# Optimization experiments

Hardware: AMD Instinct MI355X
Metric: run time of the kernel (lower is better)

Reference implementation:

```python
import jax, jax.numpy as jnp
from jax import lax
import numpy as np

B, C, H, W = 2, 256, 256, 256
NH, P = 8, 4
D = C // NH
EPS_BN = 1e-5
EPS_LN = 1e-5
EPS_ATT = 1e-6


def _maxpool(t):
    return lax.reduce_window(t, -jnp.inf, lax.max, (1, 1, P, P), (1, 1, P, P), 'VALID')


def _ln(t, g, b):  # t: [..., C]
    m = t.mean(-1, keepdims=True)
    v = ((t - m) ** 2).mean(-1, keepdims=True)
    return (t - m) * jax.lax.rsqrt(v + EPS_LN) * g + b


def _dw_bn(t, w, g, b, mu, var):  # depthwise 3x3 conv + BatchNorm2d (eval)
    y = lax.conv_general_dilated(t, w, (1, 1), ((1, 1), (1, 1)),
                                 dimension_numbers=('NCHW', 'OIHW', 'NCHW'),
                                 feature_group_count=C)
    s = g * jax.lax.rsqrt(var + EPS_BN)
    return y * s[None, :, None, None] + (b - mu * s)[None, :, None, None]


def _tokens(t, h, w):  # [N,(NH D),h,w] -> [N,(h w),NH,D]
    return t.reshape(-1, NH, D, h, w).transpose(0, 3, 4, 1, 2).reshape(-1, h * w, NH, D)


def setup_inputs() -> dict:
    key = jax.random.key(0)
    ks = jax.random.split(key, 16)
    inp = {
        'x': jax.random.normal(ks[0], (B, C, H, W), jnp.float32),
        'source': jax.random.normal(ks[1], (B, C, H, W), jnp.float32),
        'ln1_g': jnp.ones((C,), jnp.float32),
        'ln1_b': jnp.zeros((C,), jnp.float32),
        'merge_w': jax.random.normal(ks[2], (C, C), jnp.float32) * (1.0 / np.sqrt(C)),
        'mlp_w1': jax.random.normal(ks[3], (2 * C, 2 * C), jnp.float32) * (1.0 / np.sqrt(2 * C)),
        'mlp_w2': jax.random.normal(ks[4], (C, 2 * C), jnp.float32) * (1.0 / np.sqrt(2 * C)),
        'ln2_g': jnp.ones((C,), jnp.float32),
        'ln2_b': jnp.zeros((C,), jnp.float32),
    }
    for i, p in enumerate(['q', 'k', 'v']):
        kk = jax.random.split(ks[5 + i], 3)
        inp[p + '_w'] = jax.random.normal(kk[0], (C, 1, 3, 3), jnp.float32) * 0.2
        inp[p + '_bn_g'] = jnp.ones((C,), jnp.float32)
        inp[p + '_bn_b'] = jnp.zeros((C,), jnp.float32)
        inp[p + '_bn_m'] = jax.random.normal(kk[1], (C,), jnp.float32) * 0.05
        inp[p + '_bn_v'] = jax.random.uniform(kk[2], (C,), jnp.float32, 0.5, 1.5)
    return inp


def _forward(x, source, ln1_g, ln1_b,
             q_w, q_bn_g, q_bn_b, q_bn_m, q_bn_v,
             k_w, k_bn_g, k_bn_b, k_bn_m, k_bn_v,
             v_w, v_bn_g, v_bn_b, v_bn_m, v_bn_v,
             merge_w, mlp_w1, mlp_w2, ln2_g, ln2_b):
    h, w = H // P, W // P
    L = h * w
    # pre-norm after pooling (norm_before=True, max_pool path)
    q_sp = _ln(_maxpool(x).transpose(0, 2, 3, 1), ln1_g, ln1_b).transpose(0, 3, 1, 2)
    s_sp = _ln(_maxpool(source).transpose(0, 2, 3, 1), ln1_g, ln1_b).transpose(0, 3, 1, 2)
    # conv QKV projections (depthwise 3x3 + BN)
    q = _tokens(_dw_bn(q_sp, q_w, q_bn_g, q_bn_b, q_bn_m, q_bn_v), h, w)
    k = _tokens(_dw_bn(s_sp, k_w, k_bn_g, k_bn_b, k_bn_m, k_bn_v), h, w)
    v = _tokens(_dw_bn(s_sp, v_w, v_bn_g, v_bn_b, v_bn_m, v_bn_v), h, w)
    # LoFTR LinearAttention: feature map elu(x)+1
    Q = jax.nn.elu(q) + 1.0
    K = jax.nn.elu(k) + 1.0
    v_len = v.shape[1]
    KV = jnp.einsum('nshd,nshv->nhdv', K, v / v_len)
    Z = 1.0 / (jnp.einsum('nlhd,nhd->nlh', Q, K.sum(axis=1)) + EPS_ATT)
    msg = jnp.einsum('nlhd,nhdv,nlh->nlhv', Q, KV, Z) * v_len  # [N,L,NH,D]
    # merge + upsample
    msg = msg.reshape(B, L, C) @ merge_w.T
    msg = msg.reshape(B, h, w, C).transpose(0, 3, 1, 2)
    msg = jax.image.resize(msg, (B, C, H, W), method='bilinear')
    # merge-MLP + norm2 + residual
    cat = jnp.concatenate([x, msg], axis=1).transpose(0, 2, 3, 1)  # [B,H,W,2C]
    m = jax.nn.relu(cat @ mlp_w1.T) @ mlp_w2.T
    m = _ln(m, ln2_g, ln2_b).transpose(0, 3, 1, 2)
    return x + m


def reference(x, source, ln1_g, ln1_b,
              q_w, q_bn_g, q_bn_b, q_bn_m, q_bn_v,
              k_w, k_bn_g, k_bn_b, k_bn_m, k_bn_v,
              v_w, v_bn_g, v_bn_b, v_bn_m, v_bn_v,
              merge_w, mlp_w1, mlp_w2, ln2_g, ln2_b):
    return _forward(x, source, ln1_g, ln1_b,
                    q_w, q_bn_g, q_bn_b, q_bn_m, q_bn_v,
                    k_w, k_bn_g, k_bn_b, k_bn_m, k_bn_v,
                    v_w, v_bn_g, v_bn_b, v_bn_m, v_bn_v,
                    merge_w, mlp_w1, mlp_w2, ln2_g, ln2_b)
```

## Files before the change

### kernel.cpp

```cpp
#include <hip/hip_runtime.h>
#include <hip/hip_bf16.h>
#include <cstdint>


typedef __attribute__((ext_vector_type(8))) short bf16x8;
typedef __attribute__((ext_vector_type(4))) float f32x4;

#define SWZ(p, off) ((off) ^ (((p) & 7) << 4))

__device__ inline unsigned pk2bf(float a, float b) {
    unsigned ua = __builtin_bit_cast(unsigned, a);
    ua += 0x7fffu + ((ua >> 16) & 1u);
    unsigned ub = __builtin_bit_cast(unsigned, b);
    ub += 0x7fffu + ((ub >> 16) & 1u);
    return (ua >> 16) | (ub & 0xffff0000u);
}
__device__ inline float bitf(unsigned u) { return __builtin_bit_cast(float, u); }

__global__ void build_wimg(const float* __restrict__ w1, const float* __restrict__ w2,
                           uint4* __restrict__ w1img, uint4* __restrict__ w2img) {
    int idx = blockIdx.x * 256 + threadIdx.x;
    if (idx < 32768) {
        int rk = idx >> 11, jt = (idx >> 6) & 31, l = idx & 63;
        int j = jt * 16 + (l & 15);
        int k0 = rk * 32 + 8 * (l >> 4);
        const float* s = w1 + j * 512 + k0;
        uint4 pk;
        pk.x = pk2bf(s[0], s[1]); pk.y = pk2bf(s[2], s[3]);
        pk.z = pk2bf(s[4], s[5]); pk.w = pk2bf(s[6], s[7]);
        w1img[idx] = pk;
    } else {
        int id2 = idx - 32768;
        int rj = id2 >> 10, ct = (id2 >> 6) & 15, l = id2 & 63;
        int c = ct * 16 + (l & 15);
        int j0 = rj * 32 + 8 * (l >> 4);
        const float* s = w2 + c * 512 + j0;
        uint4 pk;
        pk.x = pk2bf(s[0], s[1]); pk.y = pk2bf(s[2], s[3]);
        pk.z = pk2bf(s[4], s[5]); pk.w = pk2bf(s[6], s[7]);
        w2img[id2] = pk;
    }
}

__global__ __launch_bounds__(512) void poolln_k(
    const float* __restrict__ x, const float* __restrict__ src,
    const float* __restrict__ g, const float* __restrict__ bvec,
    float* __restrict__ q_sp, float* __restrict__ s_sp) {
    extern __shared__ char smem[];
    float* tile = (float*)smem;
    float* ps = tile + 16640;
    float* pq = ps + 512;
    float* mr = pq + 512;
    float* rr = mr + 64;
    int qy = blockIdx.x, b = blockIdx.y, z = blockIdx.z;
    const float* in = z ? src : x;
    float* out = z ? s_sp : q_sp;
    int t = threadIdx.x;
    int qx = t & 63;
    int gq = t >> 6;
    for (int cc = 0; cc < 32; cc++) {
        int cl = gq + cc * 8;
        const float* rp = in + (((b * 256 + cl) * 256) + 4 * qy) * 256 + 4 * qx;
        float4 r0 = *(const float4*)(rp);
        float4 r1 = *(const float4*)(rp + 256);
        float4 r2 = *(const float4*)(rp + 512);
        float4 r3 = *(const float4*)(rp + 768);
        float m = fmaxf(fmaxf(fmaxf(r0.x, r0.y), fmaxf(r0.z, r0.w)),
                        fmaxf(fmaxf(r1.x, r1.y), fmaxf(r1.z, r1.w)));
        m = fmaxf(m, fmaxf(fmaxf(r2.x, r2.y), fmaxf(r2.z, r2.w)));
        m = fmaxf(m, fmaxf(fmaxf(r3.x, r3.y), fmaxf(r3.z, r3.w)));
        tile[cl * 65 + qx] = m;
    }
    __syncthreads();
    {
        float s = 0.f, q = 0.f;
        for (int i = 0; i < 32; i++) {
            float v = tile[(gq * 32 + i) * 65 + qx];
            s += v; q += v * v;
        }
        ps[gq * 64 + qx] = s;
        pq[gq * 64 + qx] = q;
    }
    __syncthreads();
    if (t < 64) {
        float s = 0.f, q = 0.f;
#pragma unroll
        for (int ww = 0; ww < 8; ww++) { s += ps[ww * 64 + t]; q += pq[ww * 64 + t]; }
        float mean = s * (1.f / 256.f);
        float var = q * (1.f / 256.f) - mean * mean;
        mr[t] = mean; rr[t] = rsqrtf(var + 1e-5f);
    }
    __syncthreads();
    for (int cb4 = 0; cb4 < 4; cb4++) {
#pragma unroll
        for (int kk = 0; kk < 8; kk++) {
            int cl = t & 63;
            int qxx = gq + kk * 8;
            int c = cb4 * 64 + cl;
            float v = tile[c * 65 + qxx];
            out[((b * 64 + qy) * 64 + qxx) * 256 + c] =
                (v - mr[qxx]) * rr[qxx] * g[c] + bvec[c];
        }
    }
}

__global__ void dwconv_k(const float* __restrict__ q_sp, const float* __restrict__ s_sp,
                         const float* __restrict__ qw, const float* __restrict__ qg,
                         const float* __restrict__ qb, const float* __restrict__ qm,
                         const float* __restrict__ qvar,
                         const float* __restrict__ kw, const float* __restrict__ kg,
                         const float* __restrict__ kb, const float* __restrict__ km,
                         const float* __restrict__ kvar,
                         const float* __restrict__ vw, const float* __restrict__ vg,
                         const float* __restrict__ vb, const float* __restrict__ vm,
                         const float* __restrict__ vvar,
                         float* __restrict__ qf, float* __restrict__ kf, float* __restrict__ vf) {
    int bid = blockIdx.x;
    int b = bid >> 12, l = bid & 4095, y = l >> 6, xx = l & 63;
    int c = threadIdx.x;
    float aq = 0.f, ak = 0.f, av = 0.f;
#pragma unroll
    for (int ky = 0; ky < 3; ky++) {
        int yy = y + ky - 1;
        if (yy < 0 || yy > 63) continue;
#pragma unroll
        for (int kx = 0; kx < 3; kx++) {
            int x2 = xx + kx - 1;
            if (x2 < 0 || x2 > 63) continue;
            int off = ((b * 64 + yy) * 64 + x2) * 256 + c;
            float a = q_sp[off], s = s_sp[off];
            aq += a * qw[c * 9 + ky * 3 + kx];
            ak += s * kw[c * 9 + ky * 3 + kx];
            av += s * vw[c * 9 + ky * 3 + kx];
        }
    }
    float sq = qg[c] * rsqrtf(qvar[c] + 1e-5f);
    float sk = kg[c] * rsqrtf(kvar[c] + 1e-5f);
    float sv = vg[c] * rsqrtf(vvar[c] + 1e-5f);
    float oq = aq * sq + (qb[c] - qm[c] * sq);
    float ok = ak * sk + (kb[c] - km[c] * sk);
    float ov = av * sv + (vb[c] - vm[c] * sv);
    oq = oq > 0.f ? oq + 1.f : expm1f(oq) + 1.f;
    ok = ok > 0.f ? ok + 1.f : expm1f(ok) + 1.f;
    int o = (b * 4096 + l) * 256 + c;
    qf[o] = oq; kf[o] = ok; vf[o] = ov;
}

__global__ void kv_part(const float* __restrict__ kf, const float* __restrict__ vf,
                        float* __restrict__ kvp, float* __restrict__ kspart) {
    __shared__ float red[4][1024];
    __shared__ float kred[4][32];
    int bid = blockIdx.x;
    int bnh = bid >> 4, ch = bid & 15;
    int b = bnh >> 3, nh = bnh & 7;
    int t = threadIdx.x;
    int ls = t >> 6, dkg = (t >> 3) & 7, dvg = t & 7;
    const float* kb = kf + (size_t)b * 4096 * 256 + nh * 32 + dkg * 4;
    const float* vb = vf + (size_t)b * 4096 * 256 + nh * 32 + dvg * 4;
    int l0 = ch * 256 + ls * 64;
    float4 a0 = {0,0,0,0}, a1 = a0, a2 = a0, a3 = a0, ks = a0;
    for (int l = l0; l < l0 + 64; l++) {
        float4 k4 = *(const float4*)(kb + (size_t)l * 256);
        float4 v4 = *(const float4*)(vb + (size_t)l * 256);
        a0.x += k4.x * v4.x; a0.y += k4.x * v4.y; a0.z += k4.x * v4.z; a0.w += k4.x * v4.w;
        a1.x += k4.y * v4.x; a1.y += k4.y * v4.y; a1.z += k4.y * v4.z; a1.w += k4.y * v4.w;
        a2.x += k4.z * v4.x; a2.y += k4.z * v4.y; a2.z += k4.z * v4.z; a2.w += k4.z * v4.w;
        a3.x += k4.w * v4.x; a3.y += k4.w * v4.y; a3.z += k4.w * v4.z; a3.w += k4.w * v4.w;
        ks.x += k4.x; ks.y += k4.y; ks.z += k4.z; ks.w += k4.w;
    }
    int base = dkg * 128 + dvg * 4;
    *(float4*)(&red[ls][base])      = a0;
    *(float4*)(&red[ls][base + 32]) = a1;
    *(float4*)(&red[ls][base + 64]) = a2;
    *(float4*)(&red[ls][base + 96]) = a3;
    if (dvg == 0) *(float4*)(&kred[ls][dkg * 4]) = ks;
    __syncthreads();
    for (int e = t; e < 1024; e += 256)
        kvp[bid * 1024 + e] = red[0][e] + red[1][e] + red[2][e] + red[3][e];
    if (t < 32) kspart[bid * 32 + t] = kred[0][t] + kred[1][t] + kred[2][t] + kred[3][t];
}

__global__ void kv_red(const float* __restrict__ kvp, const float* __restrict__ kspart,
                       float* __restrict__ kv, float* __restrict__ ksum) {
    int bnh = blockIdx.x;
    int t = threadIdx.x;
    for (int e = t; e < 1024; e += 256) {
        float s = 0.f;
        for (int ch = 0; ch < 16; ch++) s += kvp[(bnh * 16 + ch) * 1024 + e];
        kv[bnh * 1024 + e] = s;
    }
    if (t < 32) {
        float s = 0.f;
        for (int ch = 0; ch < 16; ch++) s += kspart[(bnh * 16 + ch) * 32 + t];
        ksum[bnh * 32 + t] = s;
    }
}

__global__ void msgmerge_k(const float* __restrict__ qf, const float* __restrict__ kv,
                           const float* __restrict__ ksum, const float* __restrict__ mw,
                           float* __restrict__ merged) {
    __shared__ float Qs[8 * 256];
    __shared__ float Ms[8 * 256];
    int bid = blockIdx.x;
    int b = bid >> 9, l0 = (bid & 511) * 8;
    int t = threadIdx.x;
#pragma unroll
    for (int tt = 0; tt < 8; tt++) Qs[tt * 256 + t] = qf[(b * 4096 + l0 + tt) * 256 + t];
    __syncthreads();
    int nh = t >> 5, dv = t & 31;
    const float* kvb = kv + (b * 8 + nh) * 1024 + dv;
    const float* ksb = ksum + (b * 8 + nh) * 32;
    float sacc[8] = {0, 0, 0, 0, 0, 0, 0, 0};
    float zacc[8] = {0, 0, 0, 0, 0, 0, 0, 0};
    for (int dk = 0; dk < 32; dk++) {
        float kvv = kvb[dk * 32];
        float ksv = ksb[dk];
#pragma unroll
        for (int tt = 0; tt < 8; tt++) {
            float qv = Qs[tt * 256 + nh * 32 + dk];
            sacc[tt] += qv * kvv;
            zacc[tt] += qv * ksv;
        }
    }
#pragma unroll
    for (int tt = 0; tt < 8; tt++) Ms[tt * 256 + t] = sacc[tt] / (zacc[tt] + 1e-6f);
    __syncthreads();
    float acc8[8] = {0, 0, 0, 0, 0, 0, 0, 0};
    const float* wrow = mw + t * 256;
    for (int c = 0; c < 256; c++) {
        float wv = wrow[c];
#pragma unroll
        for (int tt = 0; tt < 8; tt++) acc8[tt] += Ms[tt * 256 + c] * wv;
    }
#pragma unroll
    for (int tt = 0; tt < 8; tt++) merged[(b * 4096 + l0 + tt) * 256 + t] = acc8[tt];
}

__global__ __launch_bounds__(512, 4) void mlp_k(
    const float* __restrict__ x, const float* __restrict__ merged,
    const uint4* __restrict__ w1img, const uint4* __restrict__ w2img,
    const float* __restrict__ g2, const float* __restrict__ b2,
    float* __restrict__ out) {
    extern __shared__ char smem[];
    char* CATB = smem;
    float* ps = (float*)(smem + 65536);
    float* pq = ps + 512;
    float* mr = pq + 512;
    float* rr = mr + 64;
    const int t = threadIdx.x;
    const int lane = t & 63;
    const int l15 = lane & 15, l4 = lane >> 4;
    const int w = t >> 6;
    const int X0 = blockIdx.x * 64;
    const int Y = blockIdx.y;
    const int b = blockIdx.z;

    {
        const int p = lane;
        const int ch0 = w * 8;
#pragma unroll
        for (int it = 0; it < 4; it++) {
            int c0 = ch0 + it * 64;
            float v[8];
#pragma unroll
            for (int j = 0; j < 8; j++)
                v[j] = x[((b * 256 + c0 + j) * 256 + Y) * 256 + X0 + p];
            uint4 pk;
            pk.x = pk2bf(v[0], v[1]); pk.y = pk2bf(v[2], v[3]);
            pk.z = pk2bf(v[4], v[5]); pk.w = pk2bf(v[6], v[7]);
            *(uint4*)(CATB + SWZ(p, p * 1024 + c0 * 2)) = pk;
        }
        float sy = (Y - 1.5f) * 0.25f;
        int iy0 = (int)floorf(sy);
        float fy = sy - (float)iy0;
        int y0c = iy0 < 0 ? 0 : iy0;
        int y1c = (iy0 + 1) > 63 ? 63 : (iy0 + 1);
        int X = X0 + p;
        float sx = (X - 1.5f) * 0.25f;
        int ix0 = (int)floorf(sx);
        float fx = sx - (float)ix0;
        int x0c = ix0 < 0 ? 0 : ix0;
        int x1c = (ix0 + 1) > 63 ? 63 : (ix0 + 1);
        float w00 = (1.f - fy) * (1.f - fx), w01 = (1.f - fy) * fx;
        float w10 = fy * (1.f - fx), w11 = fy * fx;
        const float* m00 = merged + ((b * 64 + y0c) * 64 + x0c) * 256;
        const float* m01 = merged + ((b * 64 + y0c) * 64 + x1c) * 256;
        const float* m10 = merged + ((b * 64 + y1c) * 64 + x0c) * 256;
        const float* m11 = merged + ((b * 64 + y1c) * 64 + x1c) * 256;
#pragma unroll
        for (int it = 0; it < 4; it++) {
            int c0 = ch0 + it * 64;
            float v[8];
#pragma unroll
            for (int j = 0; j < 8; j++)
                v[j] = w00 * m00[c0 + j] + w01 * m01[c0 + j] + w10 * m10[c0 + j] + w11 * m11[c0 + j];
            uint4 pk;
            pk.x = pk2bf(v[0], v[1]); pk.y = pk2bf(v[2], v[3]);
            pk.z = pk2bf(v[4], v[5]); pk.w = pk2bf(v[6], v[7]);
            *(uint4*)(CATB + SWZ(p, p * 1024 + (256 + c0) * 2)) = pk;
        }
    }
    __syncthreads();

    f32x4 acc[4][4];
#pragma unroll
    for (int a = 0; a < 4; a++)
#pragma unroll
        for (int n = 0; n < 4; n++) acc[a][n] = (f32x4){0.f, 0.f, 0.f, 0.f};
    {
        const uint4* w1p = w1img + (w * 4) * 64 + lane;
        bf16x8 wa[4], wn[4], bfr[4];
#pragma unroll
        for (int a = 0; a < 4; a++) wa[a] = *(const bf16x8*)(w1p + a * 64);
#pragma unroll
        for (int it = 0; it < 8; it++) {
            int rk = it * 2;
#pragma unroll
            for (int a = 0; a < 4; a++) wn[a] = *(const bf16x8*)(w1p + (rk + 1) * 2048 + a * 64);
#pragma unroll
            for (int n = 0; n < 4; n++) {
                int pr = n * 16 + l15;
                bfr[n] = *(const bf16x8*)(CATB + SWZ(pr, pr * 1024 + rk * 64 + l4 * 16));
            }
#pragma unroll
            for (int a = 0; a < 4; a++)
#pragma unroll
                for (int n = 0; n < 4; n++)
                    acc[a][n] = __builtin_amdgcn_mfma_f32_16x16x32_bf16(wa[a], bfr[n], acc[a][n], 0, 0, 0);
            if (it < 7) {
#pragma unroll
                for (int a = 0; a < 4; a++) wa[a] = *(const bf16x8*)(w1p + (rk + 2) * 2048 + a * 64);
            }
#pragma unroll
            for (int n = 0; n < 4; n++) {
                int pr = n * 16 + l15;
                bfr[n] = *(const bf16x8*)(CATB + SWZ(pr, pr * 1024 + (rk + 1) * 64 + l4 * 16));
            }
#pragma unroll
            for (int a = 0; a < 4; a++)
#pragma unroll
                for (int n = 0; n < 4; n++)
                    acc[a][n] = __builtin_amdgcn_mfma_f32_16x16x32_bf16(wn[a], bfr[n], acc[a][n], 0, 0, 0);
        }
    }

    uint2 xs[8];
#pragma unroll
    for (int cc = 0; cc < 2; cc++) {
        int c0 = w * 32 + cc * 16 + l4 * 4;
#pragma unroll
        for (int n = 0; n < 4; n++) {
            int px = n * 16 + l15;
            xs[cc * 4 + n] = *(const uint2*)(CATB + SWZ(px, px * 1024 + c0 * 2));
        }
    }
    __syncthreads();

#pragma unroll
    for (int a = 0; a < 4; a++) {
        int j0 = w * 64 + a * 16 + l4 * 4;
#pragma unroll
        for (int n = 0; n < 4; n++) {
            int pr = n * 16 + l15;
            uint2 u;
            u.x = pk2bf(fmaxf(acc[a][n][0], 0.f), fmaxf(acc[a][n][1], 0.f));
            u.y = pk2bf(fmaxf(acc[a][n][2], 0.f), fmaxf(acc[a][n][3], 0.f));
            *(uint2*)(CATB + SWZ(pr, pr * 1024 + j0 * 2)) = u;
        }
    }
    __syncthreads();

    f32x4 macc[2][4];
#pragma unroll
    for (int c = 0; c < 2; c++)
#pragma unroll
        for (int n = 0; n < 4; n++) macc[c][n] = (f32x4){0.f, 0.f, 0.f, 0.f};
    {
        const uint4* w2p = w2img + (w * 2) * 64 + lane;
        bf16x8 va[2], vn[2], bfr[4];
#pragma unroll
        for (int c = 0; c < 2; c++) va[c] = *(const bf16x8*)(w2p + c * 64);
#pragma unroll
        for (int it = 0; it < 8; it++) {
            int rj = it * 2;
#pragma unroll
            for (int c = 0; c < 2; c++) vn[c] = *(const bf16x8*)(w2p + (rj + 1) * 1024 + c * 64);
#pragma unroll
            for (int n = 0; n < 4; n++) {
                int pr = n * 16 + l15;
                bfr[n] = *(const bf16x8*)(CATB + SWZ(pr, pr * 1024 + rj * 64 + l4 * 16));
            }
#pragma unroll
            for (int c = 0; c < 2; c++)
#pragma unroll
                for (int n = 0; n < 4; n++)
                    macc[c][n] = __builtin_amdgcn_mfma_f32_16x16x32_bf16(va[c], bfr[n], macc[c][n], 0, 0, 0);
            if (it < 7) {
#pragma unroll
                for (int c = 0; c < 2; c++) va[c] = *(const bf16x8*)(w2p + (rj + 2) * 1024 + c * 64);
            }
#pragma unroll
            for (int n = 0; n < 4; n++) {
                int pr = n * 16 + l15;
                bfr[n] = *(const bf16x8*)(CATB + SWZ(pr, pr * 1024 + (rj + 1) * 64 + l4 * 16));
            }
#pragma unroll
            for (int c = 0; c < 2; c++)
#pragma unroll
                for (int n = 0; n < 4; n++)
                    macc[c][n] = __builtin_amdgcn_mfma_f32_16x16x32_bf16(vn[c], bfr[n], macc[c][n], 0, 0, 0);
        }
    }

    float s[4], q[4];
#pragma unroll
    for (int n = 0; n < 4; n++) {
        float ss = 0.f, qq = 0.f;
#pragma unroll
        for (int c = 0; c < 2; c++)
#pragma unroll
            for (int r = 0; r < 4; r++) { float vv = macc[c][n][r]; ss += vv; qq += vv * vv; }
        ss += __shfl_xor(ss, 16); ss += __shfl_xor(ss, 32);
        qq += __shfl_xor(qq, 16); qq += __shfl_xor(qq, 32);
        s[n] = ss; q[n] = qq;
    }
    if (l4 == 0) {
#pragma unroll
        for (int n = 0; n < 4; n++) {
            ps[w * 64 + n * 16 + l15] = s[n];
            pq[w * 64 + n * 16 + l15] = q[n];
        }
    }
    __syncthreads();
    if (t < 64) {
        float ss = 0.f, qq = 0.f;
#pragma unroll
        for (int ww = 0; ww < 8; ww++) { ss += ps[ww * 64 + t]; qq += pq[ww * 64 + t]; }
        float mean = ss * (1.f / 256.f);
        float var = qq * (1.f / 256.f) - mean * mean;
        mr[t] = mean; rr[t] = rsqrtf(var + 1e-5f);
    }
    __syncthreads();
#pragma unroll
    for (int c = 0; c < 2; c++) {
        int cbase = w * 32 + c * 16 + l4 * 4;
        float gg[4], bb[4];
#pragma unroll
        for (int r = 0; r < 4; r++) { gg[r] = g2[cbase + r]; bb[r] = b2[cbase + r]; }
#pragma unroll
        for (int n = 0; n < 4; n++) {
            int px = n * 16 + l15;
            uint2 u = xs[c * 4 + n];
            float xr[4];
            xr[0] = bitf(u.x << 16); xr[1] = bitf(u.x & 0xffff0000u);
            xr[2] = bitf(u.y << 16); xr[3] = bitf(u.y & 0xffff0000u);
            float mean = mr[px], rs = rr[px];
#pragma unroll
            for (int r = 0; r < 4; r++) {
                out[((b * 256 + cbase + r) * 256 + Y) * 256 + X0 + px] =
                    xr[r] + (macc[c][n][r] - mean) * rs * gg[r] + bb[r];
            }
        }
    }
}

extern "C" void kernel_launch(void* const* d_in, const int* in_sizes, int n_in,
                              void* d_out, int out_size, void* d_ws, size_t ws_size,
                              hipStream_t stream) {
    const float* x       = (const float*)d_in[0];
    const float* source  = (const float*)d_in[1];
    const float* ln1_g   = (const float*)d_in[2];
    const float* ln1_b   = (const float*)d_in[3];
    const float* merge_w = (const float*)d_in[4];
    const float* mlp_w1  = (const float*)d_in[5];
    const float* mlp_w2  = (const float*)d_in[6];
    const float* ln2_g   = (const float*)d_in[7];
    const float* ln2_b   = (const float*)d_in[8];
    const float* q_w = (const float*)d_in[9];
    const float* q_bn_g = (const float*)d_in[10];
    const float* q_bn_b = (const float*)d_in[11];
    const float* q_bn_m = (const float*)d_in[12];
    const float* q_bn_v = (const float*)d_in[13];
    const float* k_w = (const float*)d_in[14];
    const float* k_bn_g = (const float*)d_in[15];
    const float* k_bn_b = (const float*)d_in[16];
    const float* k_bn_m = (const float*)d_in[17];
    const float* k_bn_v = (const float*)d_in[18];
    const float* v_w = (const float*)d_in[19];
    const float* v_bn_g = (const float*)d_in[20];
    const float* v_bn_b = (const float*)d_in[21];
    const float* v_bn_m = (const float*)d_in[22];
    const float* v_bn_v = (const float*)d_in[23];
    float* out = (float*)d_out;

    float* ws = (float*)d_ws;
    float* q_sp   = ws + 0;
    float* s_sp   = ws + 2097152;
    float* qf     = ws + 4194304;
    float* kf     = ws + 6291456;
    float* vf     = ws + 8388608;
    float* merged = ws + 10485760;
    float* kvp    = ws + 0;
    float* kspart = ws + 262144;
    float* kv     = ws + 12650496;
    float* ksum   = ws + 12666880;
    uint4* w1img  = (uint4*)((char*)d_ws + 50669568);
    uint4* w2img  = (uint4*)((char*)d_ws + 51193856);

    hipFuncSetAttribute(reinterpret_cast<const void*>(mlp_k),
                        hipFuncAttributeMaxDynamicSharedMemorySize, 70144);
    hipFuncSetAttribute(reinterpret_cast<const void*>(poolln_k),
                        hipFuncAttributeMaxDynamicSharedMemorySize, 71168);

    build_wimg<<<192, 256, 0, stream>>>(mlp_w1, mlp_w2, w1img, w2img);
    poolln_k<<<dim3(64, 2, 2), 512, 71168, stream>>>(x, source, ln1_g, ln1_b, q_sp, s_sp);
    dwconv_k<<<8192, 256, 0, stream>>>(q_sp, s_sp,
                                       q_w, q_bn_g, q_bn_b, q_bn_m, q_bn_v,
                                       k_w, k_bn_g, k_bn_b, k_bn_m, k_bn_v,
                                       v_w, v_bn_g, v_bn_b, v_bn_m, v_bn_v,
                                       qf, kf, vf);
    kv_part<<<256, 256, 0, stream>>>(kf, vf, kvp, kspart);
    kv_red<<<16, 256, 0, stream>>>(kvp, kspart, kv, ksum);
    msgmerge_k<<<1024, 256, 0, stream>>>(qf, kv, ksum, merge_w, merged);
    mlp_k<<<dim3(4, 256, 2), 512, 70144, stream>>>(x, merged, w1img, w2img, ln2_g, ln2_b, out);
}
```

Measured before the change: 415.7 us.

## Widen MLP kernel tile to 128 pixels with 1024-thread blocks

The fused MLP kernel now processes 128 pixels per block with 16 waves instead of 64 pixels with 8 waves. Waves are split into two pixel groups that share the same weight slices, so weight fragments are reused across more pixels per block. LDS per block doubles to about 140KB and the LayerNorm reduction is extended to 128 pixels. The manual double-buffered weight prefetch in both GEMM loops is replaced by a simple per-step load loop, which may expose global load latency. The launch bound of 1024 threads with a minimum of 4 blocks may also squeeze registers.

```diff
diff --git a/kernel.cpp b/kernel.cpp
--- a/kernel.cpp
+++ b/kernel.cpp
@@ -236,31 +236,32 @@
     for (int tt = 0; tt < 8; tt++) merged[(b * 4096 + l0 + tt) * 256 + t] = acc8[tt];
 }
 
-__global__ __launch_bounds__(512, 4) void mlp_k(
+__global__ __launch_bounds__(1024, 4) void mlp_k(
     const float* __restrict__ x, const float* __restrict__ merged,
     const uint4* __restrict__ w1img, const uint4* __restrict__ w2img,
     const float* __restrict__ g2, const float* __restrict__ b2,
     float* __restrict__ out) {
     extern __shared__ char smem[];
     char* CATB = smem;
-    float* ps = (float*)(smem + 65536);
-    float* pq = ps + 512;
-    float* mr = pq + 512;
-    float* rr = mr + 64;
+    float* ps = (float*)(smem + 131072);
+    float* pq = ps + 1024;
+    float* mr = pq + 1024;
+    float* rr = mr + 128;
     const int t = threadIdx.x;
     const int lane = t & 63;
     const int l15 = lane & 15, l4 = lane >> 4;
     const int w = t >> 6;
-    const int X0 = blockIdx.x * 64;
+    const int pxg = w >> 3, jg = w & 7;
+    const int X0 = blockIdx.x * 128;
     const int Y = blockIdx.y;
     const int b = blockIdx.z;
 
     {
-        const int p = lane;
-        const int ch0 = w * 8;
+        const int p = t & 127;
+        const int cg8 = t >> 7;
 #pragma unroll
         for (int it = 0; it < 4; it++) {
-            int c0 = ch0 + it * 64;
+            int c0 = cg8 * 8 + it * 64;
             float v[8];
 #pragma unroll
             for (int j = 0; j < 8; j++)
@@ -289,7 +290,7 @@
         const float* m11 = merged + ((b * 64 + y1c) * 64 + x1c) * 256;
 #pragma unroll
         for (int it = 0; it < 4; it++) {
-            int c0 = ch0 + it * 64;
+            int c0 = cg8 * 8 + it * 64;
             float v[8];
 #pragma unroll
             for (int j = 0; j < 8; j++)
@@ -308,18 +309,14 @@
 #pragma unroll
         for (int n = 0; n < 4; n++) acc[a][n] = (f32x4){0.f, 0.f, 0.f, 0.f};
     {
-        const uint4* w1p = w1img + (w * 4) * 64 + lane;
-        bf16x8 wa[4], wn[4], bfr[4];
-#pragma unroll
-        for (int a = 0; a < 4; a++) wa[a] = *(const bf16x8*)(w1p + a * 64);
-#pragma unroll
-        for (int it = 0; it < 8; it++) {
-            int rk = it * 2;
-#pragma unroll
-            for (int a = 0; a < 4; a++) wn[a] = *(const bf16x8*)(w1p + (rk + 1) * 2048 + a * 64);
+        const uint4* w1p = w1img + (jg * 4) * 64 + lane;
+        for (int rk = 0; rk < 16; rk++) {
+            bf16x8 wa[4], bfr[4];
+#pragma unroll
+            for (int a = 0; a < 4; a++) wa[a] = *(const bf16x8*)(w1p + rk * 2048 + a * 64);
 #pragma unroll
             for (int n = 0; n < 4; n++) {
-                int pr = n * 16 + l15;
+                int pr = pxg * 64 + n * 16 + l15;
                 bfr[n] = *(const bf16x8*)(CATB + SWZ(pr, pr * 1024 + rk * 64 + l4 * 16));
             }
 #pragma unroll
@@ -327,30 +324,16 @@
 #pragma unroll
                 for (int n = 0; n < 4; n++)
                     acc[a][n] = __builtin_amdgcn_mfma_f32_16x16x32_bf16(wa[a], bfr[n], acc[a][n], 0, 0, 0);
-            if (it < 7) {
-#pragma unroll
-                for (int a = 0; a < 4; a++) wa[a] = *(const bf16x8*)(w1p + (rk + 2) * 2048 + a * 64);
-            }
-#pragma unroll
-            for (int n = 0; n < 4; n++) {
-                int pr = n * 16 + l15;
-                bfr[n] = *(const bf16x8*)(CATB + SWZ(pr, pr * 1024 + (rk + 1) * 64 + l4 * 16));
-            }
-#pragma unroll
-            for (int a = 0; a < 4; a++)
-#pragma unroll
-                for (int n = 0; n < 4; n++)
-                    acc[a][n] = __builtin_amdgcn_mfma_f32_16x16x32_bf16(wn[a], bfr[n], acc[a][n], 0, 0, 0);
         }
     }
 
     uint2 xs[8];
 #pragma unroll
     for (int cc = 0; cc < 2; cc++) {
-        int c0 = w * 32 + cc * 16 + l4 * 4;
+        int c0 = jg * 32 + cc * 16 + l4 * 4;
 #pragma unroll
         for (int n = 0; n < 4; n++) {
-            int px = n * 16 + l15;
+            int px = pxg * 64 + n * 16 + l15;
             xs[cc * 4 + n] = *(const uint2*)(CATB + SWZ(px, px * 1024 + c0 * 2));
         }
     }
@@ -358,10 +341,10 @@
 
 #pragma unroll
     for (int a = 0; a < 4; a++) {
-        int j0 = w * 64 + a * 16 + l4 * 4;
+        int j0 = jg * 64 + a * 16 + l4 * 4;
 #pragma unroll
         for (int n = 0; n < 4; n++) {
-            int pr = n * 16 + l15;
+            int pr = pxg * 64 + n * 16 + l15;
             uint2 u;
             u.x = pk2bf(fmaxf(acc[a][n][0], 0.f), fmaxf(acc[a][n][1], 0.f));
             u.y = pk2bf(fmaxf(acc[a][n][2], 0.f), fmaxf(acc[a][n][3], 0.f));
@@ -376,18 +359,14 @@
 #pragma unroll
         for (int n = 0; n < 4; n++) macc[c][n] = (f32x4){0.f, 0.f, 0.f, 0.f};
     {
-        const uint4* w2p = w2img + (w * 2) * 64 + lane;
-        bf16x8 va[2], vn[2], bfr[4];
-#pragma unroll
-        for (int c = 0; c < 2; c++) va[c] = *(const bf16x8*)(w2p + c * 64);
-#pragma unroll
-        for (int it = 0; it < 8; it++) {
-            int rj = it * 2;
-#pragma unroll
-            for (int c = 0; c < 2; c++) vn[c] = *(const bf16x8*)(w2p + (rj + 1) * 1024 + c * 64);
+        const uint4* w2p = w2img + (jg * 2) * 64 + lane;
+        for (int rj = 0; rj < 16; rj++) {
+            bf16x8 va[2], bfr[4];
+#pragma unroll
+            for (int c = 0; c < 2; c++) va[c] = *(const bf16x8*)(w2p + rj * 1024 + c * 64);
 #pragma unroll
             for (int n = 0; n < 4; n++) {
-                int pr = n * 16 + l15;
+                int pr = pxg * 64 + n * 16 + l15;
                 bfr[n] = *(const bf16x8*)(CATB + SWZ(pr, pr * 1024 + rj * 64 + l4 * 16));
             }
 #pragma unroll
@@ -395,20 +374,6 @@
 #pragma unroll
                 for (int n = 0; n < 4; n++)
                     macc[c][n] = __builtin_amdgcn_mfma_f32_16x16x32_bf16(va[c], bfr[n], macc[c][n], 0, 0, 0);
-            if (it < 7) {
-#pragma unroll
-                for (int c = 0; c < 2; c++) va[c] = *(const bf16x8*)(w2p + (rj + 2) * 1024 + c * 64);
-            }
-#pragma unroll
-            for (int n = 0; n < 4; n++) {
-                int pr = n * 16 + l15;
-                bfr[n] = *(const bf16x8*)(CATB + SWZ(pr, pr * 1024 + (rj + 1) * 64 + l4 * 16));
-            }
-#pragma unroll
-            for (int c = 0; c < 2; c++)
-#pragma unroll
-                for (int n = 0; n < 4; n++)
-                    macc[c][n] = __builtin_amdgcn_mfma_f32_16x16x32_bf16(vn[c], bfr[n], macc[c][n], 0, 0, 0);
         }
     }
 
@@ -432,10 +397,14 @@
         }
     }
     __syncthreads();
-    if (t < 64) {
+    if (t < 128) {
+        int pg = t >> 6, pl = t & 63;
         float ss = 0.f, qq = 0.f;
 #pragma unroll
-        for (int ww = 0; ww < 8; ww++) { ss += ps[ww * 64 + t]; qq += pq[ww * 64 + t]; }
+        for (int ww = 0; ww < 8; ww++) {
+            ss += ps[(pg * 8 + ww) * 64 + pl];
+            qq += pq[(pg * 8 + ww) * 64 + pl];
+        }
         float mean = ss * (1.f / 256.f);
         float var = qq * (1.f / 256.f) - mean * mean;
         mr[t] = mean; rr[t] = rsqrtf(var + 1e-5f);
@@ -443,13 +412,13 @@
     __syncthreads();
 #pragma unroll
     for (int c = 0; c < 2; c++) {
-        int cbase = w * 32 + c * 16 + l4 * 4;
+        int cbase = jg * 32 + c * 16 + l4 * 4;
         float gg[4], bb[4];
 #pragma unroll
         for (int r = 0; r < 4; r++) { gg[r] = g2[cbase + r]; bb[r] = b2[cbase + r]; }
 #pragma unroll
         for (int n = 0; n < 4; n++) {
-            int px = n * 16 + l15;
+            int px = pxg * 64 + n * 16 + l15;
             uint2 u = xs[c * 4 + n];
             float xr[4];
             xr[0] = bitf(u.x << 16); xr[1] = bitf(u.x & 0xffff0000u);
@@ -508,7 +477,7 @@
     uint4* w2img  = (uint4*)((char*)d_ws + 51193856);
 
     hipFuncSetAttribute(reinterpret_cast<const void*>(mlp_k),
-                        hipFuncAttributeMaxDynamicSharedMemorySize, 70144);
+                        hipFuncAttributeMaxDynamicSharedMemorySize, 140288);
     hipFuncSetAttribute(reinterpret_cast<const void*>(poolln_k),
                         hipFuncAttributeMaxDynamicSharedMemorySize, 71168);
 
@@ -522,5 +491,5 @@
     kv_part<<<256, 256, 0, stream>>>(kf, vf, kvp, kspart);
     kv_red<<<16, 256, 0, stream>>>(kvp, kspart, kv, ksum);
     msgmerge_k<<<1024, 256, 0, stream>>>(qf, kv, ksum, merge_w, merged);
-    mlp_k<<<dim3(4, 256, 2), 512, 70144, stream>>>(x, merged, w1img, w2img, ln2_g, ln2_b, out);
-}
+    mlp_k<<<dim3(2, 256, 2), 1024, 140288, stream>>>(x, merged, w1img, w2img, ln2_g, ln2_b, out);
+}
```

Result: slower. 449.4 us (+8.1%).
